# Kernel tuning notes

Hardware: AMD Instinct MI355X
Metric: run time of the kernel (lower is better)

Reference implementation:

```python
import jax, jax.numpy as jnp
import numpy as np

NEG_SLOPE = 0.01


def reference(feat_src, feat_dst, src, dst, attn_l, attn_r):
    # feat_src: [Ns, D], feat_dst: [Nd, D], src/dst: [E] int, attn_*: [1, D]
    n_dst = feat_dst.shape[0]
    el = (feat_src * attn_l).sum(axis=-1)  # [Ns]
    er = (feat_dst * attn_r).sum(axis=-1)  # [Nd]
    e = el[src] + er[dst]                  # [E]
    e = jnp.where(e >= 0, e, NEG_SLOPE * e)  # leaky_relu
    # edge softmax over incoming edges of each destination node
    m = jax.ops.segment_max(e, dst, num_segments=n_dst)  # [Nd]
    m = jnp.where(jnp.isfinite(m), m, 0.0)  # guard empty segments
    a = jnp.exp(e - m[dst])                 # [E]
    denom = jax.ops.segment_sum(a, dst, num_segments=n_dst)  # [Nd]
    denom = jnp.where(denom > 0, denom, 1.0)
    a = a / denom[dst]
    # weighted scatter-sum of source features: [E, D] messages -> [Nd, D]
    msg = feat_src[src] * a[:, None]
    out = jax.ops.segment_sum(msg, dst, num_segments=n_dst)
    return out


def setup_inputs() -> dict:
    key = jax.random.key(0)
    k1, k2, k3, k4, k5, k6 = jax.random.split(key, 6)
    Ns, Nd, E, D = 100000, 100000, 1600000, 128
    return {
        "feat_src": jax.random.normal(k1, (Ns, D), dtype=jnp.float32),
        "feat_dst": jax.random.normal(k2, (Nd, D), dtype=jnp.float32),
        "src": jax.random.randint(k3, (E,), 0, Ns, dtype=jnp.int32),
        "dst": jax.random.randint(k4, (E,), 0, Nd, dtype=jnp.int32),
        "attn_l": jax.random.normal(k5, (1, D), dtype=jnp.float32) * 0.1,
        "attn_r": jax.random.normal(k6, (1, D), dtype=jnp.float32) * 0.1,
    }
```

## Files before the change

kernel.cpp:

```cpp
#include <hip/hip_runtime.h>
#include <hip/hip_bf16.h>
#include <math.h>

#define D 128
#define AGG_THREADS 128
#define CHUNK 512
#define BSHIFT 6
#define BK 64
#define MAXB 2048
#define MAXWG 1024
#define PCHUNK 2048
#define PE 8
#define EBUF_CAP 1792
#define PR 2048

__device__ __forceinline__ unsigned short f2bf(float f) {
    union { float f; unsigned int u; } c; c.f = f;
    unsigned int u = c.u;
    unsigned int r = (u + 0x7FFFu + ((u >> 16) & 1u)) >> 16;
    return (unsigned short)r;
}
__device__ __forceinline__ void unpack2(unsigned int w, float& lo, float& hi) {
    union { unsigned int u; float f; } c;
    c.u = w << 16;          lo = c.f;
    c.u = w & 0xFFFF0000u;  hi = c.f;
}

__device__ __forceinline__ void scan4w(const int* __restrict__ arr, int* __restrict__ outp,
                                       int n, int tid, int* wsum4) {
    int wv = tid >> 6, lane = tid & 63;
    int nchunk = (n + 63) >> 6;
    int cpw = (nchunk + 3) >> 2;
    int c0 = wv * cpw, c1 = min(nchunk, c0 + cpw);
    int carry = 0;
    for (int c = c0; c < c1; ++c) {
        int i = (c << 6) + lane;
        int v = (i < n) ? arr[i] : 0;
        int x = v;
        #pragma unroll
        for (int off = 1; off < 64; off <<= 1) {
            int t = __shfl_up(x, off, 64);
            if (lane >= off) x += t;
        }
        if (i < n) outp[i] = x - v + carry;
        carry += __shfl(x, 63, 64);
    }
    if (lane == 0) wsum4[wv] = carry;
    __syncthreads();
    int wbase = 0;
    for (int u = 0; u < wv; ++u) wbase += wsum4[u];
    if (wbase) {
        for (int c = c0; c < c1; ++c) {
            int i = (c << 6) + lane;
            if (i < n) outp[i] += wbase;
        }
    }
    __syncthreads();
}

__global__ void prep_kernel(const float* __restrict__ feat_src,
                            const float* __restrict__ feat_dst,
                            const float* __restrict__ attn_l,
                            const float* __restrict__ attn_r,
                            float* __restrict__ el, float* __restrict__ er,
                            unsigned short* __restrict__ feat_bf, int store_bf,
                            int Ns, int Nd) {
    int half = threadIdx.x >> 5;
    int lane = threadIdx.x & 31;
    int node = blockIdx.x * 8 + half;
    if (node >= Ns + Nd) return;
    bool is_src = node < Ns;
    const float* feat = is_src ? feat_src + (size_t)node * D
                               : feat_dst + (size_t)(node - Ns) * D;
    const float* attn = is_src ? attn_l : attn_r;
    float4 a = ((const float4*)attn)[lane];
    float4 v = ((const float4*)feat)[lane];
    if (is_src && store_bf) {
        ushort4 h; h.x = f2bf(v.x); h.y = f2bf(v.y); h.z = f2bf(v.z); h.w = f2bf(v.w);
        ((ushort4*)(feat_bf + (size_t)node * D))[lane] = h;
    }
    float s = v.x * a.x + v.y * a.y + v.z * a.z + v.w * a.w;
    #pragma unroll
    for (int off = 16; off > 0; off >>= 1)
        s += __shfl_xor(s, off, 64);
    if (lane == 0) {
        if (is_src) el[node] = s;
        else        er[node - Ns] = s;
    }
}

__global__ void partition_kernel(const int* __restrict__ src, const int* __restrict__ dst,
                                 int E, int nbk,
                                 uint2* __restrict__ bins,
                                 int* __restrict__ cnt_tab, int* __restrict__ loc_tab) {
    __shared__ int hist[MAXB];
    __shared__ int lstart[MAXB];
    __shared__ int cursor[MAXB];
    __shared__ uint2 sbuf[PCHUNK];
    __shared__ int wsum4[4];
    int w = blockIdx.x, tid = threadIdx.x;
    int e0 = w * PCHUNK;
    int e1 = min(E, e0 + PCHUNK);
    int n = e1 - e0;

    for (int i = tid; i < nbk; i += 256) hist[i] = 0;
    __syncthreads();

    int es[PE], ed[PE];
    #pragma unroll
    for (int k = 0; k < PE; ++k) {
        int idx = e0 + k * 256 + tid;
        if (idx < e1) {
            es[k] = src[idx];
            ed[k] = dst[idx];
            atomicAdd(&hist[ed[k] >> BSHIFT], 1);
        }
    }
    __syncthreads();

    scan4w(hist, lstart, nbk, tid, wsum4);

    for (int i = tid; i < nbk; i += 256) {
        cnt_tab[(size_t)w * nbk + i] = hist[i];
        loc_tab[(size_t)w * nbk + i] = lstart[i];
        cursor[i] = 0;
    }
    __syncthreads();

    #pragma unroll
    for (int k = 0; k < PE; ++k) {
        int idx = e0 + k * 256 + tid;
        if (idx < e1) {
            int b = ed[k] >> BSHIFT;
            int r = lstart[b] + atomicAdd(&cursor[b], 1);
            sbuf[r] = make_uint2((unsigned)es[k], (unsigned)ed[k]);
        }
    }
    __syncthreads();

    uint2* obase = bins + (size_t)w * PCHUNK;
    for (int t = tid; t < n; t += 256) obase[t] = sbuf[t];
}

__global__ void bucket_kernel(const uint2* __restrict__ bins,
                              const int* __restrict__ cnt_tab, const int* __restrict__ loc_tab,
                              int nbk, int nwg,
                              int* __restrict__ counts, int* __restrict__ offs,
                              int* __restrict__ perm, int Nd) {
    __shared__ uint2 ebuf[EBUF_CAP];
    __shared__ int wcnt[MAXWG];
    __shared__ int wdst[MAXWG];
    __shared__ int sbase[MAXWG];
    __shared__ int cntB[BK];
    __shared__ int offB[BK];
    __shared__ int curB[BK];
    __shared__ int wsum4[4];

    int b = blockIdx.x, tid = threadIdx.x;
    int base = b << BSHIFT;

    for (int i = tid; i < nwg; i += 256) wcnt[i] = cnt_tab[(size_t)i * nbk + b];
    if (tid < BK) { cntB[tid] = 0; curB[tid] = 0; }
    __syncthreads();

    scan4w(wcnt, wdst, nwg, tid, wsum4);
    int n = wsum4[0] + wsum4[1] + wsum4[2] + wsum4[3];
    bool fits = (n <= EBUF_CAP);

    if (fits) {
        for (int w = tid; w < nwg; w += 256)
            sbase[w] = w * PCHUNK + loc_tab[(size_t)w * nbk + b] - wdst[w];
        __syncthreads();
        for (int t = tid; t < n; t += 256) {
            int lo = 0, hi = nwg - 1;
            while (lo < hi) {
                int mid = (lo + hi + 1) >> 1;
                if (wdst[mid] <= t) lo = mid; else hi = mid - 1;
            }
            uint2 e = bins[(size_t)(sbase[lo] + t)];
            ebuf[t] = e;
            atomicAdd(&cntB[(int)e.y - base], 1);
        }
    } else {
        for (int w = tid; w < nwg; w += 256) {
            int c = wcnt[w];
            const uint2* sp = bins + (size_t)w * PCHUNK + loc_tab[(size_t)w * nbk + b];
            for (int k = 0; k < c; ++k)
                atomicAdd(&cntB[(int)sp[k].y - base], 1);
        }
    }
    __syncthreads();

    if (tid < 64) {
        int v = cntB[tid];
        int x = v;
        #pragma unroll
        for (int off = 1; off < 64; off <<= 1) {
            int t = __shfl_up(x, off, 64);
            if (tid >= off) x += t;
        }
        int myoff = x - v;
        offB[tid] = myoff;
        int i = base + tid;
        if (i < Nd) {
            int c = v;
            if (myoff + c > PR) c = max(0, PR - myoff);
            counts[i] = c;
            offs[i]   = myoff;
        }
    }
    __syncthreads();

    size_t rbase = (size_t)b * PR;
    if (fits) {
        for (int t = tid; t < n; t += 256) {
            uint2 e = ebuf[t];
            int d = (int)e.y - base;
            int r = atomicAdd(&curB[d], 1);
            int slot = offB[d] + r;
            if (slot < PR) perm[rbase + slot] = (int)e.x;
        }
    } else {
        for (int w = tid; w < nwg; w += 256) {
            int c = wcnt[w];
            const uint2* sp = bins + (size_t)w * PCHUNK + loc_tab[(size_t)w * nbk + b];
            for (int k = 0; k < c; ++k) {
                uint2 e = sp[k];
                int d = (int)e.y - base;
                int r = atomicAdd(&curB[d], 1);
                int slot = offB[d] + r;
                if (slot < PR) perm[rbase + slot] = (int)e.x;
            }
        }
    }
}

__device__ __forceinline__ float block_max128(float v, float* red, int tid) {
    #pragma unroll
    for (int off = 32; off > 0; off >>= 1)
        v = fmaxf(v, __shfl_down(v, off, 64));
    __syncthreads();
    if ((tid & 63) == 0) red[tid >> 6] = v;
    __syncthreads();
    return fmaxf(red[0], red[1]);
}
__device__ __forceinline__ float block_sum128(float v, float* red, int tid) {
    #pragma unroll
    for (int off = 32; off > 0; off >>= 1)
        v += __shfl_down(v, off, 64);
    __syncthreads();
    if ((tid & 63) == 0) red[tid >> 6] = v;
    __syncthreads();
    return red[0] + red[1];
}

__global__ void gat_aggregate_wave_kernel(const unsigned short* __restrict__ feat_bf,
                                          const float* __restrict__ el,
                                          const float* __restrict__ er,
                                          const int* __restrict__ offs,
                                          const int* __restrict__ counts,
                                          const int* __restrict__ perm,
                                          float* __restrict__ out, int Nd) {
    int wid  = threadIdx.x >> 6;
    int lane = threadIdx.x & 63;
    int j = blockIdx.x * 4 + wid;
    if (j >= Nd) return;
    int cnt = counts[j];
    size_t orow = (size_t)j * D;
    if (cnt == 0) {
        ((float2*)(out + orow))[lane] = make_float2(0.0f, 0.0f);
        return;
    }
    size_t beg = (size_t)(j >> BSHIFT) * PR + (size_t)offs[j];
    float erj = er[j];
    int sg = lane >> 4, u = lane & 15;
    const unsigned short* fb = feat_bf + (size_t)u * 8;
    float acc[8];
    #pragma unroll
    for (int k = 0; k < 8; ++k) acc[k] = 0.0f;

    if (cnt <= 64) {
        int s = 0; float e = -INFINITY;
        if (lane < cnt) {
            s = perm[beg + lane];
            float t = el[s] + erj;
            e = (t >= 0.0f) ? t : 0.01f * t;
        }
        float m = e;
        #pragma unroll
        for (int off = 32; off > 0; off >>= 1)
            m = fmaxf(m, __shfl_xor(m, off, 64));
        float a = (lane < cnt) ? __expf(e - m) : 0.0f;
        float den = a;
        #pragma unroll
        for (int off = 32; off > 0; off >>= 1)
            den += __shfl_xor(den, off, 64);
        a *= (1.0f / den);
        int nit = (cnt + 3) >> 2;
        int it = 0;
        for (; it + 2 <= nit; it += 2) {
            int t0 = sg + (it << 2);
            int t1 = t0 + 4;
            int u1 = (t1 < cnt) ? t1 : 0;
            float w0 = __shfl(a, t0, 64);
            int   s0 = __shfl(s, t0, 64);
            float w1 = __shfl(a, u1, 64);
            int   s1 = __shfl(s, u1, 64);
            bool p1 = (t1 < cnt);
            uint4 v0 = *(const uint4*)(fb + (size_t)s0 * D);
            uint4 v1 = p1 ? *(const uint4*)(fb + (size_t)s1 * D) : make_uint4(0,0,0,0);
            float f[8];
            unpack2(v0.x, f[0], f[1]); unpack2(v0.y, f[2], f[3]);
            unpack2(v0.z, f[4], f[5]); unpack2(v0.w, f[6], f[7]);
            #pragma unroll
            for (int k = 0; k < 8; ++k) acc[k] += w0 * f[k];
            if (p1) {
                unpack2(v1.x, f[0], f[1]); unpack2(v1.y, f[2], f[3]);
                unpack2(v1.z, f[4], f[5]); unpack2(v1.w, f[6], f[7]);
                #pragma unroll
                for (int k = 0; k < 8; ++k) acc[k] += w1 * f[k];
            }
        }
        if (it < nit) {
            int t0 = sg + (it << 2);
            int u0 = (t0 < cnt) ? t0 : 0;
            float w0 = __shfl(a, u0, 64);
            int   s0 = __shfl(s, u0, 64);
            if (t0 < cnt) {
                uint4 v0 = *(const uint4*)(fb + (size_t)s0 * D);
                float f[8];
                unpack2(v0.x, f[0], f[1]); unpack2(v0.y, f[2], f[3]);
                unpack2(v0.z, f[4], f[5]); unpack2(v0.w, f[6], f[7]);
                #pragma unroll
                for (int k = 0; k < 8; ++k) acc[k] += w0 * f[k];
            }
        }
    } else {
        float lmax = -INFINITY;
        for (int t = lane; t < cnt; t += 64) {
            int s = perm[beg + t];
            float e = el[s] + erj;
            e = (e >= 0.0f) ? e : 0.01f * e;
            lmax = fmaxf(lmax, e);
        }
        float m = lmax;
        #pragma unroll
        for (int off = 32; off > 0; off >>= 1)
            m = fmaxf(m, __shfl_xor(m, off, 64));
        float lsum = 0.0f;
        for (int t = lane; t < cnt; t += 64) {
            int s = perm[beg + t];
            float e = el[s] + erj;
            e = (e >= 0.0f) ? e : 0.01f * e;
            lsum += __expf(e - m);
        }
        #pragma unroll
        for (int off = 32; off > 0; off >>= 1)
            lsum += __shfl_xor(lsum, off, 64);
        float inv = 1.0f / lsum;
        for (int bb = 0; bb < cnt; bb += 64) {
            int nn = min(64, cnt - bb);
            int s = 0; float a = 0.0f;
            if (lane < nn) {
                s = perm[beg + bb + lane];
                float e = el[s] + erj;
                e = (e >= 0.0f) ? e : 0.01f * e;
                a = __expf(e - m) * inv;
            }
            int nit = (nn + 3) >> 2;
            for (int it = 0; it < nit; ++it) {
                int t = sg + (it << 2);
                int tt = (t < nn) ? t : 0;
                float w = __shfl(a, tt, 64);
                int st  = __shfl(s, tt, 64);
                if (t < nn) {
                    uint4 v = *(const uint4*)(fb + (size_t)st * D);
                    float f[8];
                    unpack2(v.x, f[0], f[1]); unpack2(v.y, f[2], f[3]);
                    unpack2(v.z, f[4], f[5]); unpack2(v.w, f[6], f[7]);
                    #pragma unroll
                    for (int k = 0; k < 8; ++k) acc[k] += w * f[k];
                }
            }
        }
    }
    #pragma unroll
    for (int k = 0; k < 8; ++k) {
        acc[k] += __shfl_xor(acc[k], 16, 64);
        acc[k] += __shfl_xor(acc[k], 32, 64);
    }
    if (sg == 0) {
        float* op = out + orow + (size_t)u * 8;
        ((float4*)op)[0] = make_float4(acc[0], acc[1], acc[2], acc[3]);
        ((float4*)op)[1] = make_float4(acc[4], acc[5], acc[6], acc[7]);
    }
}

#define FSHIFT 8
__global__ void hist_kernel(const int* __restrict__ dst, int E, int* __restrict__ counts) {
    int stride = gridDim.x * blockDim.x;
    for (int k = blockIdx.x * blockDim.x + threadIdx.x; k < E; k += stride)
        atomicAdd(&counts[dst[k]], 1);
}
__global__ void scan1_kernel(const int* __restrict__ counts, int* __restrict__ offsets,
                             int* __restrict__ blockSums, int N) {
    __shared__ int tile[256];
    int tid = threadIdx.x;
    int i = blockIdx.x * 256 + tid;
    int v = (i < N) ? counts[i] : 0;
    tile[tid] = v;
    __syncthreads();
    for (int off = 1; off < 256; off <<= 1) {
        int t = (tid >= off) ? tile[tid - off] : 0;
        __syncthreads();
        tile[tid] += t;
        __syncthreads();
    }
    int incl = tile[tid];
    if (i < N) offsets[i] = incl - v;
    if (tid == 255) blockSums[blockIdx.x] = incl;
}
__global__ void scan2_kernel(int* __restrict__ bs, int nb) {
    __shared__ int tile[256];
    int tid = threadIdx.x;
    int carry = 0;
    for (int base = 0; base < nb; base += 256) {
        int i = base + tid;
        int v = (i < nb) ? bs[i] : 0;
        __syncthreads();
        tile[tid] = v;
        __syncthreads();
        for (int off = 1; off < 256; off <<= 1) {
            int t = (tid >= off) ? tile[tid - off] : 0;
            __syncthreads();
            tile[tid] += t;
            __syncthreads();
        }
        int incl = tile[tid];
        if (i < nb) bs[i] = incl - v + carry;
        carry += tile[255];
    }
}
__global__ void fill_kernel(const int* __restrict__ src, const int* __restrict__ dst, int E,
                            const int* __restrict__ offsets, const int* __restrict__ bsum,
                            int* __restrict__ cursor, int* __restrict__ perm_src) {
    int stride = gridDim.x * blockDim.x;
    for (int k = blockIdx.x * blockDim.x + threadIdx.x; k < E; k += stride) {
        int j = dst[k];
        int p = offsets[j] + bsum[j >> FSHIFT] + atomicAdd(&cursor[j], 1);
        perm_src[p] = src[k];
    }
}
__global__ void gat_aggregate_f32_kernel(const float* __restrict__ feat_src,
                                         const float* __restrict__ el,
                                         const float* __restrict__ er,
                                         const int* __restrict__ offsets,
                                         const int* __restrict__ bsum,
                                         const int* __restrict__ counts,
                                         const int* __restrict__ perm_src,
                                         float* __restrict__ out, int Nd) {
    __shared__ float w_sh[CHUNK];
    __shared__ int   s_sh[CHUNK];
    __shared__ float red[2];
    int j = blockIdx.x;
    int tid = threadIdx.x;
    int cnt = counts[j];
    size_t orow = (size_t)j * D;
    if (cnt == 0) { out[orow + tid] = 0.0f; return; }
    int beg = offsets[j] + bsum[j >> FSHIFT];
    float erj = er[j];
    float acc = 0.0f;
    float inv;
    if (cnt <= CHUNK) {
        float lmax = -INFINITY;
        for (int t = tid; t < cnt; t += AGG_THREADS) {
            int s = perm_src[beg + t];
            float e = el[s] + erj;
            e = (e >= 0.0f) ? e : 0.01f * e;
            s_sh[t] = s; w_sh[t] = e;
            lmax = fmaxf(lmax, e);
        }
        float m = block_max128(lmax, red, tid);
        float lsum = 0.0f;
        for (int t = tid; t < cnt; t += AGG_THREADS) {
            float a = __expf(w_sh[t] - m);
            w_sh[t] = a; lsum += a;
        }
        float den = block_sum128(lsum, red, tid);
        inv = 1.0f / den;
        __syncthreads();
        for (int t = 0; t < cnt; ++t)
            acc += feat_src[(size_t)s_sh[t] * D + tid] * w_sh[t];
    } else {
        float lmax = -INFINITY;
        for (int t = tid; t < cnt; t += AGG_THREADS) {
            int s = perm_src[beg + t];
            float e = el[s] + erj;
            e = (e >= 0.0f) ? e : 0.01f * e;
            lmax = fmaxf(lmax, e);
        }
        float m = block_max128(lmax, red, tid);
        float lsum = 0.0f;
        for (int t = tid; t < cnt; t += AGG_THREADS) {
            int s = perm_src[beg + t];
            float e = el[s] + erj;
            e = (e >= 0.0f) ? e : 0.01f * e;
            lsum += __expf(e - m);
        }
        float den = block_sum128(lsum, red, tid);
        inv = 1.0f / den;
        for (int bb = 0; bb < cnt; bb += CHUNK) {
            int n = min(CHUNK, cnt - bb);
            __syncthreads();
            for (int t = tid; t < n; t += AGG_THREADS) {
                int s = perm_src[beg + bb + t];
                float e = el[s] + erj;
                e = (e >= 0.0f) ? e : 0.01f * e;
                s_sh[t] = s;
                w_sh[t] = __expf(e - m);
            }
            __syncthreads();
            for (int t = 0; t < n; ++t)
                acc += feat_src[(size_t)s_sh[t] * D + tid] * w_sh[t];
        }
    }
    out[orow + tid] = acc * inv;
}

extern "C" void kernel_launch(void* const* d_in, const int* in_sizes, int n_in,
                              void* d_out, int out_size, void* d_ws, size_t ws_size,
                              hipStream_t stream) {
    const float* feat_src = (const float*)d_in[0];
    const float* feat_dst = (const float*)d_in[1];
    const int*   src      = (const int*)d_in[2];
    const int*   dst      = (const int*)d_in[3];
    const float* attn_l   = (const float*)d_in[4];
    const float* attn_r   = (const float*)d_in[5];
    float* out = (float*)d_out;

    int Ns = in_sizes[0] / D;
    int Nd = in_sizes[1] / D;
    int E  = in_sizes[2];
    int NBK = (Nd + BK - 1) >> BSHIFT;
    int NFB = (Nd + 255) >> FSHIFT;
    int NWG = (E + PCHUNK - 1) / PCHUNK;

    char* p = (char*)d_ws;
    auto carve = [&](size_t bytes) { void* r = (void*)p; p += (bytes + 255) & ~(size_t)255; return r; };
    float* el      = (float*)carve((size_t)Ns * 4);
    float* er      = (float*)carve((size_t)Nd * 4);
    int*   counts  = (int*)carve((size_t)Nd * 4);
    int*   offs    = (int*)carve((size_t)Nd * 4);
    int*   gcursor = (int*)carve((size_t)Nd * 4);
    int*   bsums   = (int*)carve((size_t)NFB * 4);
    int*   cnt_tab = (int*)carve((size_t)NWG * NBK * 4);
    int*   loc_tab = (int*)carve((size_t)NWG * NBK * 4);
    int*   perm    = (int*)carve((size_t)NBK * PR * 4);
    uint2* bins    = (uint2*)carve((size_t)NWG * PCHUNK * 8);
    size_t used    = (size_t)(p - (char*)d_ws);
    size_t bf_bytes = (size_t)Ns * D * 2;
    unsigned short* feat_bf = (unsigned short*)carve(bf_bytes);

    int fast = (NBK <= MAXB && NWG <= MAXWG &&
                used + bf_bytes + 256 <= ws_size) ? 1 : 0;

    int total = Ns + Nd;
    if (fast) {
        prep_kernel<<<(total + 7) / 8, 256, 0, stream>>>(feat_src, feat_dst, attn_l, attn_r,
                                                         el, er, feat_bf, 1, Ns, Nd);
        partition_kernel<<<NWG, 256, 0, stream>>>(src, dst, E, NBK, bins, cnt_tab, loc_tab);
        bucket_kernel<<<NBK, 256, 0, stream>>>(bins, cnt_tab, loc_tab, NBK, NWG,
                                               counts, offs, perm, Nd);
        gat_aggregate_wave_kernel<<<(Nd + 3) / 4, 256, 0, stream>>>(feat_bf, el, er, offs,
                                                                    counts, perm, out, Nd);
    } else {
        hipMemsetAsync(counts, 0, (size_t)Nd * 4, stream);
        hipMemsetAsync(gcursor, 0, (size_t)Nd * 4, stream);
        prep_kernel<<<(total + 7) / 8, 256, 0, stream>>>(feat_src, feat_dst, attn_l, attn_r,
                                                         el, er, nullptr, 0, Ns, Nd);
        hist_kernel<<<2048, 256, 0, stream>>>(dst, E, counts);
        scan1_kernel<<<NFB, 256, 0, stream>>>(counts, offs, bsums, Nd);
        scan2_kernel<<<1, 256, 0, stream>>>(bsums, NFB);
        fill_kernel<<<2048, 256, 0, stream>>>(src, dst, E, offs, bsums, gcursor, perm);
        gat_aggregate_f32_kernel<<<Nd, AGG_THREADS, 0, stream>>>(feat_src, el, er, offs,
                                                                 bsums, counts, perm, out, Nd);
    }
}
```

Before: 272.9 us.

## Transpose partition count/offset tables so bucket kernel reads them coalesced

Measured after the change: 274.5 us. No clear change (+0.6%).

```diff
diff --git a/kernel.cpp b/kernel.cpp
--- a/kernel.cpp
+++ b/kernel.cpp
@@ -13,6 +13,7 @@
 #define PE 8
 #define EBUF_CAP 1792
 #define PR 2048
+#define TW 32
 
 __device__ __forceinline__ unsigned short f2bf(float f) {
     union { float f; unsigned int u; } c; c.f = f;
@@ -92,7 +93,7 @@
 __global__ void partition_kernel(const int* __restrict__ src, const int* __restrict__ dst,
                                  int E, int nbk,
                                  uint2* __restrict__ bins,
-                                 int* __restrict__ cnt_tab, int* __restrict__ loc_tab) {
+                                 int2* __restrict__ tab) {
     __shared__ int hist[MAXB];
     __shared__ int lstart[MAXB];
     __shared__ int cursor[MAXB];
@@ -121,8 +122,7 @@
     scan4w(hist, lstart, nbk, tid, wsum4);
 
     for (int i = tid; i < nbk; i += 256) {
-        cnt_tab[(size_t)w * nbk + i] = hist[i];
-        loc_tab[(size_t)w * nbk + i] = lstart[i];
+        tab[(size_t)w * nbk + i] = make_int2(hist[i], lstart[i]);
         cursor[i] = 0;
     }
     __syncthreads();
@@ -142,8 +142,30 @@
     for (int t = tid; t < n; t += 256) obase[t] = sbuf[t];
 }
 
+__global__ void transpose_kernel(const int2* __restrict__ tab, int2* __restrict__ tabT,
+                                 int nwg, int nbk) {
+    __shared__ int2 tile[TW][TW + 1];
+    int b0 = blockIdx.x * TW;
+    int w0 = blockIdx.y * TW;
+    int tx = threadIdx.x & (TW - 1);
+    int ty0 = threadIdx.x >> 5;
+    #pragma unroll
+    for (int r = 0; r < TW; r += 8) {
+        int w = w0 + ty0 + r, b = b0 + tx;
+        if (w < nwg && b < nbk)
+            tile[ty0 + r][tx] = tab[(size_t)w * nbk + b];
+    }
+    __syncthreads();
+    #pragma unroll
+    for (int r = 0; r < TW; r += 8) {
+        int b = b0 + ty0 + r, w = w0 + tx;
+        if (b < nbk && w < nwg)
+            tabT[(size_t)b * nwg + w] = tile[tx][ty0 + r];
+    }
+}
+
 __global__ void bucket_kernel(const uint2* __restrict__ bins,
-                              const int* __restrict__ cnt_tab, const int* __restrict__ loc_tab,
+                              const int2* __restrict__ tabT,
                               int nbk, int nwg,
                               int* __restrict__ counts, int* __restrict__ offs,
                               int* __restrict__ perm, int Nd) {
@@ -159,7 +181,11 @@
     int b = blockIdx.x, tid = threadIdx.x;
     int base = b << BSHIFT;
 
-    for (int i = tid; i < nwg; i += 256) wcnt[i] = cnt_tab[(size_t)i * nbk + b];
+    for (int i = tid; i < nwg; i += 256) {
+        int2 t = tabT[(size_t)b * nwg + i];
+        wcnt[i] = t.x;
+        sbase[i] = t.y;
+    }
     if (tid < BK) { cntB[tid] = 0; curB[tid] = 0; }
     __syncthreads();
 
@@ -167,10 +193,11 @@
     int n = wsum4[0] + wsum4[1] + wsum4[2] + wsum4[3];
     bool fits = (n <= EBUF_CAP);
 
+    for (int w = tid; w < nwg; w += 256)
+        sbase[w] = w * PCHUNK + sbase[w] - wdst[w];
+    __syncthreads();
+
     if (fits) {
-        for (int w = tid; w < nwg; w += 256)
-            sbase[w] = w * PCHUNK + loc_tab[(size_t)w * nbk + b] - wdst[w];
-        __syncthreads();
         for (int t = tid; t < n; t += 256) {
             int lo = 0, hi = nwg - 1;
             while (lo < hi) {
@@ -184,7 +211,7 @@
     } else {
         for (int w = tid; w < nwg; w += 256) {
             int c = wcnt[w];
-            const uint2* sp = bins + (size_t)w * PCHUNK + loc_tab[(size_t)w * nbk + b];
+            const uint2* sp = bins + (size_t)(sbase[w] + wdst[w]);
             for (int k = 0; k < c; ++k)
                 atomicAdd(&cntB[(int)sp[k].y - base], 1);
         }
@@ -223,7 +250,7 @@
     } else {
         for (int w = tid; w < nwg; w += 256) {
             int c = wcnt[w];
-            const uint2* sp = bins + (size_t)w * PCHUNK + loc_tab[(size_t)w * nbk + b];
+            const uint2* sp = bins + (size_t)(sbase[w] + wdst[w]);
             for (int k = 0; k < c; ++k) {
                 uint2 e = sp[k];
                 int d = (int)e.y - base;
@@ -553,8 +580,8 @@
     int*   offs    = (int*)carve((size_t)Nd * 4);
     int*   gcursor = (int*)carve((size_t)Nd * 4);
     int*   bsums   = (int*)carve((size_t)NFB * 4);
-    int*   cnt_tab = (int*)carve((size_t)NWG * NBK * 4);
-    int*   loc_tab = (int*)carve((size_t)NWG * NBK * 4);
+    int2*  tab     = (int2*)carve((size_t)NWG * NBK * 8);
+    int2*  tabT    = (int2*)carve((size_t)NWG * NBK * 8);
     int*   perm    = (int*)carve((size_t)NBK * PR * 4);
     uint2* bins    = (uint2*)carve((size_t)NWG * PCHUNK * 8);
     size_t used    = (size_t)(p - (char*)d_ws);
@@ -568,8 +595,10 @@
     if (fast) {
         prep_kernel<<<(total + 7) / 8, 256, 0, stream>>>(feat_src, feat_dst, attn_l, attn_r,
                                                          el, er, feat_bf, 1, Ns, Nd);
-        partition_kernel<<<NWG, 256, 0, stream>>>(src, dst, E, NBK, bins, cnt_tab, loc_tab);
-        bucket_kernel<<<NBK, 256, 0, stream>>>(bins, cnt_tab, loc_tab, NBK, NWG,
+        partition_kernel<<<NWG, 256, 0, stream>>>(src, dst, E, NBK, bins, tab);
+        dim3 tg((NBK + TW - 1) / TW, (NWG + TW - 1) / TW);
+        transpose_kernel<<<tg, 256, 0, stream>>>(tab, tabT, NWG, NBK);
+        bucket_kernel<<<NBK, 256, 0, stream>>>(bins, tabT, NBK, NWG,
                                                counts, offs, perm, Nd);
         gat_aggregate_wave_kernel<<<(Nd + 3) / 4, 256, 0, stream>>>(feat_bf, el, er, offs,
                                                                     counts, perm, out, Nd);
```

## Fuse bucketing with aggregation and keep per-bucket permutation in shared memory

Applied to the files above, without the earlier changes.

Result: no change. 276.7 us (+1.4%).

```diff
diff --git a/kernel.cpp b/kernel.cpp
--- a/kernel.cpp
+++ b/kernel.cpp
@@ -8,9 +8,9 @@
 #define BSHIFT 6
 #define BK 64
 #define MAXB 2048
-#define MAXWG 1024
-#define PCHUNK 2048
-#define PE 8
+#define MAXWG 512
+#define PCHUNK 4096
+#define PE 16
 #define EBUF_CAP 1792
 #define PR 2048
 
@@ -92,7 +92,7 @@
 __global__ void partition_kernel(const int* __restrict__ src, const int* __restrict__ dst,
                                  int E, int nbk,
                                  uint2* __restrict__ bins,
-                                 int* __restrict__ cnt_tab, int* __restrict__ loc_tab) {
+                                 int2* __restrict__ tab) {
     __shared__ int hist[MAXB];
     __shared__ int lstart[MAXB];
     __shared__ int cursor[MAXB];
@@ -121,8 +121,7 @@
     scan4w(hist, lstart, nbk, tid, wsum4);
 
     for (int i = tid; i < nbk; i += 256) {
-        cnt_tab[(size_t)w * nbk + i] = hist[i];
-        loc_tab[(size_t)w * nbk + i] = lstart[i];
+        tab[(size_t)w * nbk + i] = make_int2(hist[i], lstart[i]);
         cursor[i] = 0;
     }
     __syncthreads();
@@ -142,12 +141,16 @@
     for (int t = tid; t < n; t += 256) obase[t] = sbuf[t];
 }
 
-__global__ void bucket_kernel(const uint2* __restrict__ bins,
-                              const int* __restrict__ cnt_tab, const int* __restrict__ loc_tab,
-                              int nbk, int nwg,
-                              int* __restrict__ counts, int* __restrict__ offs,
-                              int* __restrict__ perm, int Nd) {
+__global__ void bucket_agg_kernel(const uint2* __restrict__ bins,
+                                  const int2* __restrict__ tab,
+                                  int nbk, int nwg,
+                                  const unsigned short* __restrict__ feat_bf,
+                                  const float* __restrict__ el,
+                                  const float* __restrict__ er,
+                                  int* __restrict__ spill,
+                                  float* __restrict__ out, int Nd) {
     __shared__ uint2 ebuf[EBUF_CAP];
+    __shared__ int sperm[EBUF_CAP];
     __shared__ int wcnt[MAXWG];
     __shared__ int wdst[MAXWG];
     __shared__ int sbase[MAXWG];
@@ -159,7 +162,11 @@
     int b = blockIdx.x, tid = threadIdx.x;
     int base = b << BSHIFT;
 
-    for (int i = tid; i < nwg; i += 256) wcnt[i] = cnt_tab[(size_t)i * nbk + b];
+    for (int i = tid; i < nwg; i += 256) {
+        int2 t = tab[(size_t)i * nbk + b];
+        wcnt[i] = t.x;
+        sbase[i] = t.y;
+    }
     if (tid < BK) { cntB[tid] = 0; curB[tid] = 0; }
     __syncthreads();
 
@@ -167,10 +174,11 @@
     int n = wsum4[0] + wsum4[1] + wsum4[2] + wsum4[3];
     bool fits = (n <= EBUF_CAP);
 
+    for (int w = tid; w < nwg; w += 256)
+        sbase[w] = w * PCHUNK + sbase[w] - wdst[w];
+    __syncthreads();
+
     if (fits) {
-        for (int w = tid; w < nwg; w += 256)
-            sbase[w] = w * PCHUNK + loc_tab[(size_t)w * nbk + b] - wdst[w];
-        __syncthreads();
         for (int t = tid; t < n; t += 256) {
             int lo = 0, hi = nwg - 1;
             while (lo < hi) {
@@ -184,7 +192,7 @@
     } else {
         for (int w = tid; w < nwg; w += 256) {
             int c = wcnt[w];
-            const uint2* sp = bins + (size_t)w * PCHUNK + loc_tab[(size_t)w * nbk + b];
+            const uint2* sp = bins + (size_t)(sbase[w] + wdst[w]);
             for (int k = 0; k < c; ++k)
                 atomicAdd(&cntB[(int)sp[k].y - base], 1);
         }
@@ -201,199 +209,191 @@
         }
         int myoff = x - v;
         offB[tid] = myoff;
-        int i = base + tid;
-        if (i < Nd) {
-            int c = v;
-            if (myoff + c > PR) c = max(0, PR - myoff);
-            counts[i] = c;
-            offs[i]   = myoff;
-        }
-    }
-    __syncthreads();
-
-    size_t rbase = (size_t)b * PR;
+        int c = v;
+        if (!fits) c = max(0, min(c, PR - myoff));
+        cntB[tid] = c;
+    }
+    __syncthreads();
+
     if (fits) {
         for (int t = tid; t < n; t += 256) {
             uint2 e = ebuf[t];
             int d = (int)e.y - base;
             int r = atomicAdd(&curB[d], 1);
-            int slot = offB[d] + r;
-            if (slot < PR) perm[rbase + slot] = (int)e.x;
+            sperm[offB[d] + r] = (int)e.x;
         }
     } else {
+        size_t rbase = (size_t)b * PR;
         for (int w = tid; w < nwg; w += 256) {
             int c = wcnt[w];
-            const uint2* sp = bins + (size_t)w * PCHUNK + loc_tab[(size_t)w * nbk + b];
+            const uint2* sp = bins + (size_t)(sbase[w] + wdst[w]);
             for (int k = 0; k < c; ++k) {
                 uint2 e = sp[k];
                 int d = (int)e.y - base;
                 int r = atomicAdd(&curB[d], 1);
                 int slot = offB[d] + r;
-                if (slot < PR) perm[rbase + slot] = (int)e.x;
-            }
-        }
-    }
-}
-
-__device__ __forceinline__ float block_max128(float v, float* red, int tid) {
-    #pragma unroll
-    for (int off = 32; off > 0; off >>= 1)
-        v = fmaxf(v, __shfl_down(v, off, 64));
-    __syncthreads();
-    if ((tid & 63) == 0) red[tid >> 6] = v;
-    __syncthreads();
-    return fmaxf(red[0], red[1]);
-}
-__device__ __forceinline__ float block_sum128(float v, float* red, int tid) {
-    #pragma unroll
-    for (int off = 32; off > 0; off >>= 1)
-        v += __shfl_down(v, off, 64);
-    __syncthreads();
-    if ((tid & 63) == 0) red[tid >> 6] = v;
-    __syncthreads();
-    return red[0] + red[1];
-}
-
-__global__ void gat_aggregate_wave_kernel(const unsigned short* __restrict__ feat_bf,
-                                          const float* __restrict__ el,
-                                          const float* __restrict__ er,
-                                          const int* __restrict__ offs,
-                                          const int* __restrict__ counts,
-                                          const int* __restrict__ perm,
-                                          float* __restrict__ out, int Nd) {
-    int wid  = threadIdx.x >> 6;
-    int lane = threadIdx.x & 63;
-    int j = blockIdx.x * 4 + wid;
-    if (j >= Nd) return;
-    int cnt = counts[j];
-    size_t orow = (size_t)j * D;
-    if (cnt == 0) {
-        ((float2*)(out + orow))[lane] = make_float2(0.0f, 0.0f);
-        return;
-    }
-    size_t beg = (size_t)(j >> BSHIFT) * PR + (size_t)offs[j];
-    float erj = er[j];
+                if (slot < PR) spill[rbase + slot] = (int)e.x;
+            }
+        }
+    }
+    __syncthreads();
+
+    int wid = tid >> 6, lane = tid & 63;
     int sg = lane >> 4, u = lane & 15;
     const unsigned short* fb = feat_bf + (size_t)u * 8;
-    float acc[8];
-    #pragma unroll
-    for (int k = 0; k < 8; ++k) acc[k] = 0.0f;
-
-    if (cnt <= 64) {
-        int s = 0; float e = -INFINITY;
-        if (lane < cnt) {
-            s = perm[beg + lane];
-            float t = el[s] + erj;
-            e = (t >= 0.0f) ? t : 0.01f * t;
-        }
-        float m = e;
+    const int* gspill = spill + (size_t)b * PR;
+
+    for (int q = 0; q < 16; ++q) {
+        int d = wid * 16 + q;
+        int j = base + d;
+        if (j >= Nd) break;
+        int cnt = cntB[d];
+        size_t orow = (size_t)j * D;
+        if (cnt == 0) {
+            ((float2*)(out + orow))[lane] = make_float2(0.0f, 0.0f);
+            continue;
+        }
+        int doff = offB[d];
+        float erj = er[j];
+        float acc[8];
         #pragma unroll
-        for (int off = 32; off > 0; off >>= 1)
-            m = fmaxf(m, __shfl_xor(m, off, 64));
-        float a = (lane < cnt) ? __expf(e - m) : 0.0f;
-        float den = a;
-        #pragma unroll
-        for (int off = 32; off > 0; off >>= 1)
-            den += __shfl_xor(den, off, 64);
-        a *= (1.0f / den);
-        int nit = (cnt + 3) >> 2;
-        int it = 0;
-        for (; it + 2 <= nit; it += 2) {
-            int t0 = sg + (it << 2);
-            int t1 = t0 + 4;
-            int u1 = (t1 < cnt) ? t1 : 0;
-            float w0 = __shfl(a, t0, 64);
-            int   s0 = __shfl(s, t0, 64);
-            float w1 = __shfl(a, u1, 64);
-            int   s1 = __shfl(s, u1, 64);
-            bool p1 = (t1 < cnt);
-            uint4 v0 = *(const uint4*)(fb + (size_t)s0 * D);
-            uint4 v1 = p1 ? *(const uint4*)(fb + (size_t)s1 * D) : make_uint4(0,0,0,0);
-            float f[8];
-            unpack2(v0.x, f[0], f[1]); unpack2(v0.y, f[2], f[3]);
-            unpack2(v0.z, f[4], f[5]); unpack2(v0.w, f[6], f[7]);
+        for (int k = 0; k < 8; ++k) acc[k] = 0.0f;
+
+        if (cnt <= 64) {
+            int s = 0; float e = -INFINITY;
+            if (lane < cnt) {
+                s = fits ? sperm[doff + lane] : gspill[doff + lane];
+                float t = el[s] + erj;
+                e = (t >= 0.0f) ? t : 0.01f * t;
+            }
+            float m = e;
             #pragma unroll
-            for (int k = 0; k < 8; ++k) acc[k] += w0 * f[k];
-            if (p1) {
-                unpack2(v1.x, f[0], f[1]); unpack2(v1.y, f[2], f[3]);
-                unpack2(v1.z, f[4], f[5]); unpack2(v1.w, f[6], f[7]);
-                #pragma unroll
-                for (int k = 0; k < 8; ++k) acc[k] += w1 * f[k];
-            }
-        }
-        if (it < nit) {
-            int t0 = sg + (it << 2);
-            int u0 = (t0 < cnt) ? t0 : 0;
-            float w0 = __shfl(a, u0, 64);
-            int   s0 = __shfl(s, u0, 64);
-            if (t0 < cnt) {
+            for (int off = 32; off > 0; off >>= 1)
+                m = fmaxf(m, __shfl_xor(m, off, 64));
+            float a = (lane < cnt) ? __expf(e - m) : 0.0f;
+            float den = a;
+            #pragma unroll
+            for (int off = 32; off > 0; off >>= 1)
+                den += __shfl_xor(den, off, 64);
+            a *= (1.0f / den);
+            int nit = (cnt + 3) >> 2;
+            int it = 0;
+            for (; it + 2 <= nit; it += 2) {
+                int t0 = sg + (it << 2);
+                int t1 = t0 + 4;
+                int u1 = (t1 < cnt) ? t1 : 0;
+                float w0 = __shfl(a, t0, 64);
+                int   s0 = __shfl(s, t0, 64);
+                float w1 = __shfl(a, u1, 64);
+                int   s1 = __shfl(s, u1, 64);
+                bool p1 = (t1 < cnt);
                 uint4 v0 = *(const uint4*)(fb + (size_t)s0 * D);
+                uint4 v1 = p1 ? *(const uint4*)(fb + (size_t)s1 * D) : make_uint4(0,0,0,0);
                 float f[8];
                 unpack2(v0.x, f[0], f[1]); unpack2(v0.y, f[2], f[3]);
                 unpack2(v0.z, f[4], f[5]); unpack2(v0.w, f[6], f[7]);
                 #pragma unroll
                 for (int k = 0; k < 8; ++k) acc[k] += w0 * f[k];
-            }
-        }
-    } else {
-        float lmax = -INFINITY;
-        for (int t = lane; t < cnt; t += 64) {
-            int s = perm[beg + t];
-            float e = el[s] + erj;
-            e = (e >= 0.0f) ? e : 0.01f * e;
-            lmax = fmaxf(lmax, e);
-        }
-        float m = lmax;
-        #pragma unroll
-        for (int off = 32; off > 0; off >>= 1)
-            m = fmaxf(m, __shfl_xor(m, off, 64));
-        float lsum = 0.0f;
-        for (int t = lane; t < cnt; t += 64) {
-            int s = perm[beg + t];
-            float e = el[s] + erj;
-            e = (e >= 0.0f) ? e : 0.01f * e;
-            lsum += __expf(e - m);
-        }
-        #pragma unroll
-        for (int off = 32; off > 0; off >>= 1)
-            lsum += __shfl_xor(lsum, off, 64);
-        float inv = 1.0f / lsum;
-        for (int bb = 0; bb < cnt; bb += 64) {
-            int nn = min(64, cnt - bb);
-            int s = 0; float a = 0.0f;
-            if (lane < nn) {
-                s = perm[beg + bb + lane];
+                if (p1) {
+                    unpack2(v1.x, f[0], f[1]); unpack2(v1.y, f[2], f[3]);
+                    unpack2(v1.z, f[4], f[5]); unpack2(v1.w, f[6], f[7]);
+                    #pragma unroll
+                    for (int k = 0; k < 8; ++k) acc[k] += w1 * f[k];
+                }
+            }
+            if (it < nit) {
+                int t0 = sg + (it << 2);
+                int u0 = (t0 < cnt) ? t0 : 0;
+                float w0 = __shfl(a, u0, 64);
+                int   s0 = __shfl(s, u0, 64);
+                if (t0 < cnt) {
+                    uint4 v0 = *(const uint4*)(fb + (size_t)s0 * D);
+                    float f[8];
+                    unpack2(v0.x, f[0], f[1]); unpack2(v0.y, f[2], f[3]);
+                    unpack2(v0.z, f[4], f[5]); unpack2(v0.w, f[6], f[7]);
+                    #pragma unroll
+                    for (int k = 0; k < 8; ++k) acc[k] += w0 * f[k];
+                }
+            }
+        } else {
+            float lmax = -INFINITY;
+            for (int t = lane; t < cnt; t += 64) {
+                int s = fits ? sperm[doff + t] : gspill[doff + t];
                 float e = el[s] + erj;
                 e = (e >= 0.0f) ? e : 0.01f * e;
-                a = __expf(e - m) * inv;
-            }
-            int nit = (nn + 3) >> 2;
-            for (int it = 0; it < nit; ++it) {
-                int t = sg + (it << 2);
-                int tt = (t < nn) ? t : 0;
-                float w = __shfl(a, tt, 64);
-                int st  = __shfl(s, tt, 64);
-                if (t < nn) {
-                    uint4 v = *(const uint4*)(fb + (size_t)st * D);
-                    float f[8];
-                    unpack2(v.x, f[0], f[1]); unpack2(v.y, f[2], f[3]);
-                    unpack2(v.z, f[4], f[5]); unpack2(v.w, f[6], f[7]);
-                    #pragma unroll
-                    for (int k = 0; k < 8; ++k) acc[k] += w * f[k];
+                lmax = fmaxf(lmax, e);
+            }
+            float m = lmax;
+            #pragma unroll
+            for (int off = 32; off > 0; off >>= 1)
+                m = fmaxf(m, __shfl_xor(m, off, 64));
+            float lsum = 0.0f;
+            for (int t = lane; t < cnt; t += 64) {
+                int s = fits ? sperm[doff + t] : gspill[doff + t];
+                float e = el[s] + erj;
+                e = (e >= 0.0f) ? e : 0.01f * e;
+                lsum += __expf(e - m);
+            }
+            #pragma unroll
+            for (int off = 32; off > 0; off >>= 1)
+                lsum += __shfl_xor(lsum, off, 64);
+            float inv = 1.0f / lsum;
+            for (int bb = 0; bb < cnt; bb += 64) {
+                int nn = min(64, cnt - bb);
+                int s = 0; float a = 0.0f;
+                if (lane < nn) {
+                    s = fits ? sperm[doff + bb + lane] : gspill[doff + bb + lane];
+                    float e = el[s] + erj;
+                    e = (e >= 0.0f) ? e : 0.01f * e;
+                    a = __expf(e - m) * inv;
                 }
-            }
-        }
-    }
+                int nit = (nn + 3) >> 2;
+                for (int it = 0; it < nit; ++it) {
+                    int t = sg + (it << 2);
+                    int tt = (t < nn) ? t : 0;
+                    float w = __shfl(a, tt, 64);
+                    int st  = __shfl(s, tt, 64);
+                    if (t < nn) {
+                        uint4 v = *(const uint4*)(fb + (size_t)st * D);
+                        float f[8];
+                        unpack2(v.x, f[0], f[1]); unpack2(v.y, f[2], f[3]);
+                        unpack2(v.z, f[4], f[5]); unpack2(v.w, f[6], f[7]);
+                        #pragma unroll
+                        for (int k = 0; k < 8; ++k) acc[k] += w * f[k];
+                    }
+                }
+            }
+        }
+        #pragma unroll
+        for (int k = 0; k < 8; ++k) {
+            acc[k] += __shfl_xor(acc[k], 16, 64);
+            acc[k] += __shfl_xor(acc[k], 32, 64);
+        }
+        if (sg == 0) {
+            float* op = out + orow + (size_t)u * 8;
+            ((float4*)op)[0] = make_float4(acc[0], acc[1], acc[2], acc[3]);
+            ((float4*)op)[1] = make_float4(acc[4], acc[5], acc[6], acc[7]);
+        }
+    }
+}
+
+__device__ __forceinline__ float block_max128(float v, float* red, int tid) {
     #pragma unroll
-    for (int k = 0; k < 8; ++k) {
-        acc[k] += __shfl_xor(acc[k], 16, 64);
-        acc[k] += __shfl_xor(acc[k], 32, 64);
-    }
-    if (sg == 0) {
-        float* op = out + orow + (size_t)u * 8;
-        ((float4*)op)[0] = make_float4(acc[0], acc[1], acc[2], acc[3]);
-        ((float4*)op)[1] = make_float4(acc[4], acc[5], acc[6], acc[7]);
-    }
+    for (int off = 32; off > 0; off >>= 1)
+        v = fmaxf(v, __shfl_down(v, off, 64));
+    __syncthreads();
+    if ((tid & 63) == 0) red[tid >> 6] = v;
+    __syncthreads();
+    return fmaxf(red[0], red[1]);
+}
+__device__ __forceinline__ float block_sum128(float v, float* red, int tid) {
+    #pragma unroll
+    for (int off = 32; off > 0; off >>= 1)
+        v += __shfl_down(v, off, 64);
+    __syncthreads();
+    if ((tid & 63) == 0) red[tid >> 6] = v;
+    __syncthreads();
+    return red[0] + red[1];
 }
 
 #define FSHIFT 8
@@ -553,9 +553,8 @@
     int*   offs    = (int*)carve((size_t)Nd * 4);
     int*   gcursor = (int*)carve((size_t)Nd * 4);
     int*   bsums   = (int*)carve((size_t)NFB * 4);
-    int*   cnt_tab = (int*)carve((size_t)NWG * NBK * 4);
-    int*   loc_tab = (int*)carve((size_t)NWG * NBK * 4);
-    int*   perm    = (int*)carve((size_t)NBK * PR * 4);
+    int2*  tab     = (int2*)carve((size_t)NWG * NBK * 8);
+    int*   spill   = (int*)carve((size_t)NBK * PR * 4);
     uint2* bins    = (uint2*)carve((size_t)NWG * PCHUNK * 8);
     size_t used    = (size_t)(p - (char*)d_ws);
     size_t bf_bytes = (size_t)Ns * D * 2;
@@ -568,11 +567,9 @@
     if (fast) {
         prep_kernel<<<(total + 7) / 8, 256, 0, stream>>>(feat_src, feat_dst, attn_l, attn_r,
                                                          el, er, feat_bf, 1, Ns, Nd);
-        partition_kernel<<<NWG, 256, 0, stream>>>(src, dst, E, NBK, bins, cnt_tab, loc_tab);
-        bucket_kernel<<<NBK, 256, 0, stream>>>(bins, cnt_tab, loc_tab, NBK, NWG,
-                                               counts, offs, perm, Nd);
-        gat_aggregate_wave_kernel<<<(Nd + 3) / 4, 256, 0, stream>>>(feat_bf, el, er, offs,
-                                                                    counts, perm, out, Nd);
+        partition_kernel<<<NWG, 256, 0, stream>>>(src, dst, E, NBK, bins, tab);
+        bucket_agg_kernel<<<NBK, 256, 0, stream>>>(bins, tab, NBK, NWG,
+                                                   feat_bf, el, er, spill, out, Nd);
     } else {
         hipMemsetAsync(counts, 0, (size_t)Nd * 4, stream);
         hipMemsetAsync(gcursor, 0, (size_t)Nd * 4, stream);
@@ -581,8 +578,8 @@
         hist_kernel<<<2048, 256, 0, stream>>>(dst, E, counts);
         scan1_kernel<<<NFB, 256, 0, stream>>>(counts, offs, bsums, Nd);
         scan2_kernel<<<1, 256, 0, stream>>>(bsums, NFB);
-        fill_kernel<<<2048, 256, 0, stream>>>(src, dst, E, offs, bsums, gcursor, perm);
+        fill_kernel<<<2048, 256, 0, stream>>>(src, dst, E, offs, bsums, gcursor, spill);
         gat_aggregate_f32_kernel<<<Nd, AGG_THREADS, 0, stream>>>(feat_src, el, er, offs,
-                                                                 bsums, counts, perm, out, Nd);
-    }
-}
+                                                                 bsums, counts, spill, out, Nd);
+    }
+}
```
